# Performance work log

Measured on AMD Instinct MI355X. Metric: run time of the kernel, lower is better.

## Reference

```python
import jax, jax.numpy as jnp
import numpy as np

H = 128
M = 50000
L = 400000
EPS = 1e-9


def setup_inputs() -> dict:
    key = jax.random.key(0)
    ks = jax.random.split(key, 24)
    d = {
        'x_emb': jax.random.normal(ks[0], (M, H), jnp.float32),
        'child_h': jax.random.normal(ks[1], (M, H), jnp.float32),
        'child_c': jax.random.normal(ks[2], (M, H), jnp.float32),
        'pair_cand_idx': jax.random.randint(ks[3], (L,), 0, M, jnp.int32),
        'pair_child_idx': jax.random.randint(ks[4], (L,), 0, M, jnp.int32),
    }
    s = 1.0 / np.sqrt(H)
    names = ['Wi_w', 'Ui_w', 'Wf_w', 'Uf_w', 'Wo_w', 'Uo_w', 'Wc_w', 'Uc_w', 'Wa_w', 'Ua_w']
    for i, n in enumerate(names):
        d[n] = jax.random.uniform(ks[5 + i], (H, H), jnp.float32, -s, s)
    for i, n in enumerate(['Wi_b', 'Wf_b', 'Wo_b', 'Wc_b', 'Wa_b']):
        d[n] = jax.random.uniform(ks[15 + i], (H,), jnp.float32, -s, s)
    d['v_w'] = jax.random.uniform(ks[20], (H,), jnp.float32, -s, s)
    return d


def reference(x_emb, child_h, child_c, pair_cand_idx, pair_child_idx,
              Wi_w, Ui_w, Wf_w, Uf_w, Wo_w, Uo_w, Wc_w, Uc_w, Wa_w, Ua_w,
              Wi_b, Wf_b, Wo_b, Wc_b, Wa_b, v_w):
    m = x_emb.shape[0]
    ci, chi = pair_cand_idx, pair_child_idx

    # --- segment attention (torch version runs under no_grad) ---
    Ah = child_h @ Wa_w.T + Wa_b          # [M,H]
    Bx = x_emb @ Ua_w.T                   # [M,H]
    e = jnp.tanh(Ah[chi] + Bx[ci]) @ v_w  # [L]
    seg_max = jax.ops.segment_max(e, ci, num_segments=m)
    x_exp = jnp.exp(e - seg_max[ci])
    seg_sum = jax.ops.segment_sum(x_exp, ci, num_segments=m) + EPS
    attn = x_exp / seg_sum[ci]            # [L]
    h_hat = jax.ops.segment_sum(attn[:, None] * child_h[chi], ci, num_segments=m)  # [M,H]

    # --- tree-LSTM gates ---
    i_j = jax.nn.sigmoid(x_emb @ Wi_w.T + Wi_b + h_hat @ Ui_w.T)
    Wfx = x_emb @ Wf_w.T + Wf_b
    Ufh = child_h @ Uf_w.T
    f_pair = jax.nn.sigmoid(Wfx[ci] + Ufh[chi])                       # [L,H]
    sum_f_c = jax.ops.segment_sum(f_pair * child_c[chi], ci, num_segments=m)
    c_t = jnp.tanh(x_emb @ Wc_w.T + Wc_b + h_hat @ Uc_w.T)
    c = i_j * c_t + sum_f_c
    o_j = jax.nn.sigmoid(x_emb @ Wo_w.T + Wo_b + h_hat @ Uo_w.T)
    h = o_j * jnp.tanh(c)
    return (h, c)
```

## Files before the change

### kernel.cpp

```cpp
#include <hip/hip_runtime.h>
#include <cstdint>
#include <cstddef>

#define H 128
#define PSTRIDE 512

typedef __bf16 v8bf __attribute__((ext_vector_type(8)));
typedef __bf16 v4bf __attribute__((ext_vector_type(4)));
typedef float  v4f  __attribute__((ext_vector_type(4)));

__device__ __forceinline__ float ftanh(float x) {
    return 1.f - 2.f / (1.f + __expf(2.f * x));
}
__device__ __forceinline__ float fsigm(float x) {
    return 1.f / (1.f + __expf(-x));
}

struct MatDesc {
    const __bf16* A;
    int           lda;
    const __bf16* Wb;
    const float*  bias;
    __bf16*       C;
    int           ldc;
};
struct MatBatch { MatDesc m[7]; };
struct WPtrs { const float* w[10]; };

__global__ __launch_bounds__(256) void prep_k(WPtrs wp, __bf16* __restrict__ Wb,
                                              const float* __restrict__ x,
                                              const float* __restrict__ chh,
                                              const float* __restrict__ chc,
                                              __bf16* __restrict__ xe,
                                              __bf16* __restrict__ P,
                                              const int* __restrict__ ci,
                                              int* __restrict__ counts,
                                              int MH4, int L) {
    int tid = blockIdx.x * 256 + threadIdx.x;
    if (tid < 40960) {
        int mat = tid >> 12;
        int off = (tid & 4095) << 2;
        v4f a = *(const v4f*)(wp.w[mat] + off);
        v4bf b;
#pragma unroll
        for (int k = 0; k < 4; ++k) b[k] = (__bf16)a[k];
        *(v4bf*)(Wb + mat * 16384 + off) = b;
        return;
    }
    int i = tid - 40960;
    if (i < MH4) {
        v4f a = ((const v4f*)x)[i];
        v4f b = ((const v4f*)chh)[i];
        v4f c = ((const v4f*)chc)[i];
        v4bf ab, bb, cb;
#pragma unroll
        for (int k = 0; k < 4; ++k) {
            ab[k] = (__bf16)a[k]; bb[k] = (__bf16)b[k]; cb[k] = (__bf16)c[k];
        }
        ((v4bf*)xe)[i] = ab;
        int m = i >> 5;
        int q = (i & 31) << 2;
        __bf16* prow = P + (size_t)m * PSTRIDE + q;
        *(v4bf*)prow = bb;
        *(v4bf*)(prow + H) = cb;
        return;
    }
    int l = i - MH4;
    if (l < L) atomicAdd(&counts[ci[l]], 1);
}

__global__ __launch_bounds__(256) void gemm_batch(MatBatch batch, int M) {
    const MatDesc d = batch.m[blockIdx.y];
    __shared__ __bf16 wlds[H][H + 8];

    for (int t = threadIdx.x; t < 2048; t += 256) {
        int n = t >> 4;
        int k = (t & 15) << 3;
        *(v8bf*)&wlds[n][k] = *(const v8bf*)(d.Wb + n * H + k);
    }
    __syncthreads();

    const int wave = threadIdx.x >> 6;
    const int lane = threadIdx.x & 63;
    const int quad = lane >> 4;
    const int l16  = lane & 15;
    const int r0   = blockIdx.x * 128 + wave * 32;

    v4f acc0[8], acc1[8];
#pragma unroll
    for (int nt = 0; nt < 8; ++nt) {
        acc0[nt] = (v4f){0.f, 0.f, 0.f, 0.f};
        acc1[nt] = (v4f){0.f, 0.f, 0.f, 0.f};
    }

    const __bf16* ar0 = d.A + (size_t)(r0 + l16) * d.lda + quad * 8;
    const __bf16* ar1 = d.A + (size_t)(r0 + 16 + l16) * d.lda + quad * 8;
#pragma unroll
    for (int k0 = 0; k0 < H; k0 += 32) {
        v8bf a0 = *(const v8bf*)(ar0 + k0);
        v8bf a1 = *(const v8bf*)(ar1 + k0);
#pragma unroll
        for (int nt = 0; nt < 8; ++nt) {
            v8bf b = *(const v8bf*)(&wlds[nt * 16 + l16][k0 + quad * 8]);
            acc0[nt] = __builtin_amdgcn_mfma_f32_16x16x32_bf16(a0, b, acc0[nt], 0, 0, 0);
            acc1[nt] = __builtin_amdgcn_mfma_f32_16x16x32_bf16(a1, b, acc1[nt], 0, 0, 0);
        }
    }

#pragma unroll
    for (int nt = 0; nt < 8; ++nt) {
        int n = nt * 16 + l16;
        float bia = d.bias ? d.bias[n] : 0.f;
#pragma unroll
        for (int r = 0; r < 4; ++r) {
            int m0 = r0 + quad * 4 + r;
            int m1 = m0 + 16;
            if (m0 < M) d.C[(size_t)m0 * d.ldc + n] = (__bf16)(acc0[nt][r] + bia);
            if (m1 < M) d.C[(size_t)m1 * d.ldc + n] = (__bf16)(acc1[nt][r] + bia);
        }
    }
}

__global__ __launch_bounds__(1024) void scan_local(const int* __restrict__ counts,
                                                   int* __restrict__ excl,
                                                   int* __restrict__ bsums, int M) {
    __shared__ int s[1024];
    int tid = threadIdx.x;
    int idx = blockIdx.x * 1024 + tid;
    int v = (idx < M) ? counts[idx] : 0;
    s[tid] = v;
    __syncthreads();
    for (int off = 1; off < 1024; off <<= 1) {
        int t = (tid >= off) ? s[tid - off] : 0;
        __syncthreads();
        s[tid] += t;
        __syncthreads();
    }
    if (idx < M) excl[idx] = s[tid] - v;
    if (tid == 1023) bsums[blockIdx.x] = s[1023];
}

__global__ __launch_bounds__(1024) void scan_fused(int* __restrict__ rowptr,
                                                   int* __restrict__ cursor,
                                                   const int* __restrict__ bsums,
                                                   const int* __restrict__ counts,
                                                   int M, int nb) {
    __shared__ int s[1024];
    int t = threadIdx.x, b = blockIdx.x;
    int v = (t < nb) ? bsums[t] : 0;
    s[t] = v;
    __syncthreads();
    for (int off = 1; off < 1024; off <<= 1) {
        int tt = (t >= off) ? s[t - off] : 0;
        __syncthreads();
        s[t] += tt;
        __syncthreads();
    }
    int boff = (b == 0) ? 0 : s[b - 1];
    int idx = b * 1024 + t;
    if (idx < M) {
        int val = rowptr[idx] + boff;
        rowptr[idx] = val;
        cursor[idx] = val;
        if (idx == M - 1) rowptr[M] = val + counts[M - 1];
    }
}

__global__ __launch_bounds__(256) void scatter_k(const int* __restrict__ ci,
                                                 const int* __restrict__ chi,
                                                 int* __restrict__ cursor,
                                                 int* __restrict__ payload, int L) {
    int l = blockIdx.x * 256 + threadIdx.x;
    if (l < L) {
        int pos = atomicAdd(&cursor[ci[l]], 1);
        payload[pos] = chi[l];
    }
}

__global__ __launch_bounds__(128) void segment_fused(const int* __restrict__ rowptr,
                                                     const int* __restrict__ payload,
                                                     const float* __restrict__ vw,
                                                     const __bf16* __restrict__ Bx,
                                                     const __bf16* __restrict__ Wfx,
                                                     const __bf16* __restrict__ P,
                                                     __bf16* __restrict__ hhat,
                                                     float* __restrict__ sumfc, int M) {
    int wl   = threadIdx.x & 63;
    int half = wl & 32;
    int l32  = wl & 31;
    int m = blockIdx.x * 4 + (threadIdx.x >> 5);
    if (m >= M) return;
    int start = rowptr[m], deg = rowptr[m + 1] - start;
    int h = l32 << 2;

    v4bf bx4 = *(const v4bf*)(Bx + (size_t)m * H + h);
    v4bf wf4 = *(const v4bf*)(Wfx + (size_t)m * H + h);
    v4f  vv  = *(const v4f*)(vw + h);
    float bxf[4], wff[4];
#pragma unroll
    for (int k = 0; k < 4; ++k) { bxf[k] = (float)bx4[k]; wff[k] = (float)wf4[k]; }

    int pl0 = (l32 < deg) ? payload[start + l32] : 0;
    int pl1 = (32 + l32 < deg) ? payload[start + 32 + l32] : 0;

    int jcap = deg < 64 ? deg : 64;
    float e0 = 0.f, e1 = 0.f, denom = 0.f;

    for (int j = 0; j < jcap; ++j) {
        int cj = __shfl((j & 32) ? pl1 : pl0, half | (j & 31), 64);
        v4bf a4 = *(const v4bf*)(P + (size_t)cj * PSTRIDE + 3 * H + h);
        float s = 0.f;
#pragma unroll
        for (int k = 0; k < 4; ++k) s += ftanh((float)a4[k] + bxf[k]) * vv[k];
        s += __shfl_xor(s, 1);
        s += __shfl_xor(s, 2);
        s += __shfl_xor(s, 4);
        s += __shfl_xor(s, 8);
        s += __shfl_xor(s, 16);
        float ex = __expf(s);
        denom += ex;
        if (l32 == (j & 31)) { if (j & 32) e1 = ex; else e0 = ex; }
    }
    for (int j = 64; j < deg; ++j) {
        int cj = payload[start + j];
        v4bf a4 = *(const v4bf*)(P + (size_t)cj * PSTRIDE + 3 * H + h);
        float s = 0.f;
#pragma unroll
        for (int k = 0; k < 4; ++k) s += ftanh((float)a4[k] + bxf[k]) * vv[k];
        s += __shfl_xor(s, 1);
        s += __shfl_xor(s, 2);
        s += __shfl_xor(s, 4);
        s += __shfl_xor(s, 8);
        s += __shfl_xor(s, 16);
        denom += __expf(s);
    }
    float inv = 1.f / (denom + 1e-9f);

    float acch[4] = {0.f, 0.f, 0.f, 0.f};
    float accf[4] = {0.f, 0.f, 0.f, 0.f};
#pragma unroll 2
    for (int j = 0; j < jcap; ++j) {
        int src = half | (j & 31);
        int   cj = __shfl((j & 32) ? pl1 : pl0, src, 64);
        float ex = __shfl((j & 32) ? e1 : e0, src, 64);
        float a = ex * inv;
        const __bf16* pb = P + (size_t)cj * PSTRIDE + h;
        v4bf h4 = *(const v4bf*)pb;
        v4bf c4 = *(const v4bf*)(pb + H);
        v4bf u4 = *(const v4bf*)(pb + 2 * H);
#pragma unroll
        for (int k = 0; k < 4; ++k) {
            acch[k] += a * (float)h4[k];
            accf[k] += fsigm(wff[k] + (float)u4[k]) * (float)c4[k];
        }
    }
    for (int j = 64; j < deg; ++j) {
        int cj = payload[start + j];
        const __bf16* pb = P + (size_t)cj * PSTRIDE + h;
        v4bf a4 = *(const v4bf*)(pb + 3 * H);
        float s = 0.f;
#pragma unroll
        for (int k = 0; k < 4; ++k) s += ftanh((float)a4[k] + bxf[k]) * vv[k];
        s += __shfl_xor(s, 1);
        s += __shfl_xor(s, 2);
        s += __shfl_xor(s, 4);
        s += __shfl_xor(s, 8);
        s += __shfl_xor(s, 16);
        float a = __expf(s) * inv;
        v4bf h4 = *(const v4bf*)pb;
        v4bf c4 = *(const v4bf*)(pb + H);
        v4bf u4 = *(const v4bf*)(pb + 2 * H);
#pragma unroll
        for (int k = 0; k < 4; ++k) {
            acch[k] += a * (float)h4[k];
            accf[k] += fsigm(wff[k] + (float)u4[k]) * (float)c4[k];
        }
    }

    v4bf hb;
    v4f sf;
#pragma unroll
    for (int k = 0; k < 4; ++k) { hb[k] = (__bf16)acch[k]; sf[k] = accf[k]; }
    *(v4bf*)(hhat + (size_t)m * H + h) = hb;
    *(v4f*)(sumfc + (size_t)m * H + h) = sf;
}

__global__ __launch_bounds__(256) void final_k(const __bf16* __restrict__ Xi, const __bf16* __restrict__ Hi,
                                               const __bf16* __restrict__ Xc, const __bf16* __restrict__ Hc,
                                               const __bf16* __restrict__ Xo, const __bf16* __restrict__ Ho,
                                               const float* __restrict__ sumfc,
                                               float* __restrict__ out, int MH4, int MH) {
    int i = blockIdx.x * 256 + threadIdx.x;
    if (i >= MH4) return;
    v4bf xi = ((const v4bf*)Xi)[i], hi = ((const v4bf*)Hi)[i];
    v4bf xc = ((const v4bf*)Xc)[i], hc = ((const v4bf*)Hc)[i];
    v4bf xo = ((const v4bf*)Xo)[i], ho = ((const v4bf*)Ho)[i];
    v4f sf = ((const v4f*)sumfc)[i];
    v4f hout, cout;
#pragma unroll
    for (int k = 0; k < 4; ++k) {
        float ig = fsigm((float)xi[k] + (float)hi[k]);
        float ct = ftanh((float)xc[k] + (float)hc[k]);
        float og = fsigm((float)xo[k] + (float)ho[k]);
        float c = ig * ct + sf[k];
        cout[k] = c;
        hout[k] = og * ftanh(c);
    }
    ((v4f*)out)[i] = hout;
    ((v4f*)(out + MH))[i] = cout;
}

extern "C" void kernel_launch(void* const* d_in, const int* in_sizes, int n_in,
                              void* d_out, int out_size, void* d_ws, size_t ws_size,
                              hipStream_t stream) {
    const float* x_emb   = (const float*)d_in[0];
    const float* child_h = (const float*)d_in[1];
    const float* child_c = (const float*)d_in[2];
    const int*   ci      = (const int*)d_in[3];
    const int*   chi     = (const int*)d_in[4];
    const float* Wi_b = (const float*)d_in[15];
    const float* Wf_b = (const float*)d_in[16];
    const float* Wo_b = (const float*)d_in[17];
    const float* Wc_b = (const float*)d_in[18];
    const float* Wa_b = (const float*)d_in[19];
    const float* vw   = (const float*)d_in[20];

    const int M    = in_sizes[0] / H;
    const int L    = in_sizes[3];
    const int Mpad = (M + 127) & ~127;
    const int MH   = M * H;
    const int MH4  = MH / 4;

    char* p = (char*)d_ws;
    auto alloc = [&](size_t bytes) {
        char* r = p;
        p += (bytes + 255) & ~(size_t)255;
        return (void*)r;
    };
    size_t bfbytes = (size_t)Mpad * H * sizeof(__bf16);
    __bf16* xe16   = (__bf16*)alloc(bfbytes);
    __bf16* P      = (__bf16*)alloc((size_t)Mpad * PSTRIDE * sizeof(__bf16));
    __bf16* hhat16 = (__bf16*)alloc(bfbytes);
    __bf16* Bx16   = (__bf16*)alloc(bfbytes);
    __bf16* Wfx16  = (__bf16*)alloc(bfbytes);
    __bf16* Xi16   = (__bf16*)alloc(bfbytes);
    __bf16* Xc16   = (__bf16*)alloc(bfbytes);
    __bf16* Xo16   = (__bf16*)alloc(bfbytes);
    __bf16* Wb     = (__bf16*)alloc(10 * 16384 * sizeof(__bf16));
    float* sumfc   = (float*)alloc((size_t)MH * 4);
    int*   payload = (int*)alloc((size_t)L * 4);
    int*   counts  = (int*)alloc((size_t)M * 4);
    int*   rowptr  = (int*)alloc((size_t)(M + 1) * 4);
    int*   cursor  = (int*)alloc((size_t)M * 4);
    int*   bsums   = (int*)alloc(1024 * 4);
    __bf16* Hi16 = Bx16;
    __bf16* Hc16 = Wfx16;
    __bf16* Ho16 = P;

    hipMemsetAsync(counts, 0, (size_t)M * 4, stream);

    WPtrs wp;
    for (int k = 0; k < 10; ++k) wp.w[k] = (const float*)d_in[5 + k];
    int prep_items = 40960 + MH4 + L;
    prep_k<<<(prep_items + 255) / 256, 256, 0, stream>>>(wp, Wb, x_emb, child_h, child_c,
                                                         xe16, P, ci, counts, MH4, L);

    const __bf16* Wi = Wb + 0 * 16384;
    const __bf16* Ui = Wb + 1 * 16384;
    const __bf16* Wf = Wb + 2 * 16384;
    const __bf16* Uf = Wb + 3 * 16384;
    const __bf16* Wo = Wb + 4 * 16384;
    const __bf16* Uo = Wb + 5 * 16384;
    const __bf16* Wc = Wb + 6 * 16384;
    const __bf16* Uc = Wb + 7 * 16384;
    const __bf16* Wa = Wb + 8 * 16384;
    const __bf16* Ua = Wb + 9 * 16384;

    MatBatch ba{};
    ba.m[0] = MatDesc{P,    PSTRIDE, Wa, Wa_b,    P + 3 * H, PSTRIDE};
    ba.m[1] = MatDesc{xe16, H,       Ua, nullptr, Bx16,      H};
    ba.m[2] = MatDesc{xe16, H,       Wf, Wf_b,    Wfx16,     H};
    ba.m[3] = MatDesc{P,    PSTRIDE, Uf, nullptr, P + 2 * H, PSTRIDE};
    ba.m[4] = MatDesc{xe16, H,       Wi, Wi_b,    Xi16,      H};
    ba.m[5] = MatDesc{xe16, H,       Wc, Wc_b,    Xc16,      H};
    ba.m[6] = MatDesc{xe16, H,       Wo, Wo_b,    Xo16,      H};
    dim3 gA(Mpad / 128, 7);
    gemm_batch<<<gA, 256, 0, stream>>>(ba, M);

    int nb = (M + 1023) / 1024;
    scan_local<<<nb, 1024, 0, stream>>>(counts, rowptr, bsums, M);
    scan_fused<<<nb, 1024, 0, stream>>>(rowptr, cursor, bsums, counts, M, nb);

    scatter_k<<<(L + 255) / 256, 256, 0, stream>>>(ci, chi, cursor, payload, L);

    segment_fused<<<(M + 3) / 4, 128, 0, stream>>>(rowptr, payload, vw, Bx16, Wfx16, P,
                                                   hhat16, sumfc, M);

    MatBatch bb{};
    bb.m[0] = MatDesc{hhat16, H, Ui, nullptr, Hi16, H};
    bb.m[1] = MatDesc{hhat16, H, Uc, nullptr, Hc16, H};
    bb.m[2] = MatDesc{hhat16, H, Uo, nullptr, Ho16, H};
    dim3 gB(Mpad / 128, 3);
    gemm_batch<<<gB, 256, 0, stream>>>(bb, M);

    final_k<<<(MH4 + 255) / 256, 256, 0, stream>>>(Xi16, Hi16, Xc16, Hc16, Xo16, Ho16, sumfc,
                                                   (float*)d_out, MH4, MH);
}
```

Measured before the change: 402.0 us.

## Share A tiles across grouped GEMMs and process two children per wave in segment kernel

The batched GEMM now groups all matrices that share an input. Each block loads its A rows into registers once and loops over several weight matrices, double-buffering the next weight in LDS, instead of reloading A for every matrix in a separate block. The segment attention kernel now has each half-wave of 16 lanes handle a different child with 8-wide bf16 loads, so two pairs are processed per iteration. The half-wave partial sums are combined with a cross-half shuffle at the end. This cuts redundant A traffic and serial iteration count, at the cost of fewer GEMM blocks (less parallelism), more registers, and masked wasted work when the degree is odd.

```diff
diff --git a/kernel.cpp b/kernel.cpp
--- a/kernel.cpp
+++ b/kernel.cpp
@@ -16,15 +16,16 @@
     return 1.f / (1.f + __expf(-x));
 }
 
-struct MatDesc {
+struct GDesc {
     const __bf16* A;
     int           lda;
-    const __bf16* Wb;
-    const float*  bias;
-    __bf16*       C;
-    int           ldc;
+    int           nm;
+    const __bf16* W[5];
+    const float*  bias[5];
+    __bf16*       C[5];
+    int           ldc[5];
 };
-struct MatBatch { MatDesc m[7]; };
+struct GBatch { GDesc g[2]; };
 struct WPtrs { const float* w[10]; };
 
 __global__ __launch_bounds__(256) void prep_k(WPtrs wp, __bf16* __restrict__ Wb,
@@ -69,16 +70,9 @@
     if (l < L) atomicAdd(&counts[ci[l]], 1);
 }
 
-__global__ __launch_bounds__(256) void gemm_batch(MatBatch batch, int M) {
-    const MatDesc d = batch.m[blockIdx.y];
-    __shared__ __bf16 wlds[H][H + 8];
-
-    for (int t = threadIdx.x; t < 2048; t += 256) {
-        int n = t >> 4;
-        int k = (t & 15) << 3;
-        *(v8bf*)&wlds[n][k] = *(const v8bf*)(d.Wb + n * H + k);
-    }
-    __syncthreads();
+__global__ __launch_bounds__(256) void gemm_group(GBatch gb, int M) {
+    const GDesc d = gb.g[blockIdx.y];
+    __shared__ __bf16 wlds[2][H][H + 8];
 
     const int wave = threadIdx.x >> 6;
     const int lane = threadIdx.x & 63;
@@ -86,38 +80,74 @@
     const int l16  = lane & 15;
     const int r0   = blockIdx.x * 128 + wave * 32;
 
-    v4f acc0[8], acc1[8];
-#pragma unroll
-    for (int nt = 0; nt < 8; ++nt) {
-        acc0[nt] = (v4f){0.f, 0.f, 0.f, 0.f};
-        acc1[nt] = (v4f){0.f, 0.f, 0.f, 0.f};
-    }
-
+#pragma unroll
+    for (int i = 0; i < 8; ++i) {
+        int c = threadIdx.x + 256 * i;
+        int n = c >> 4, k = (c & 15) << 3;
+        *(v8bf*)&wlds[0][n][k] = *(const v8bf*)(d.W[0] + n * H + k);
+    }
+
+    v8bf afr0[4], afr1[4];
     const __bf16* ar0 = d.A + (size_t)(r0 + l16) * d.lda + quad * 8;
-    const __bf16* ar1 = d.A + (size_t)(r0 + 16 + l16) * d.lda + quad * 8;
-#pragma unroll
-    for (int k0 = 0; k0 < H; k0 += 32) {
-        v8bf a0 = *(const v8bf*)(ar0 + k0);
-        v8bf a1 = *(const v8bf*)(ar1 + k0);
+    const __bf16* ar1 = ar0 + (size_t)16 * d.lda;
+#pragma unroll
+    for (int kc = 0; kc < 4; ++kc) {
+        afr0[kc] = *(const v8bf*)(ar0 + kc * 32);
+        afr1[kc] = *(const v8bf*)(ar1 + kc * 32);
+    }
+    __syncthreads();
+
+    for (int mat = 0; mat < d.nm; ++mat) {
+        int cur = mat & 1;
+        v8bf pf[8];
+        if (mat + 1 < d.nm) {
+#pragma unroll
+            for (int i = 0; i < 8; ++i) {
+                int c = threadIdx.x + 256 * i;
+                pf[i] = *(const v8bf*)(d.W[mat + 1] + (c >> 4) * H + ((c & 15) << 3));
+            }
+        }
+
+        v4f acc0[8], acc1[8];
 #pragma unroll
         for (int nt = 0; nt < 8; ++nt) {
-            v8bf b = *(const v8bf*)(&wlds[nt * 16 + l16][k0 + quad * 8]);
-            acc0[nt] = __builtin_amdgcn_mfma_f32_16x16x32_bf16(a0, b, acc0[nt], 0, 0, 0);
-            acc1[nt] = __builtin_amdgcn_mfma_f32_16x16x32_bf16(a1, b, acc1[nt], 0, 0, 0);
-        }
-    }
-
-#pragma unroll
-    for (int nt = 0; nt < 8; ++nt) {
-        int n = nt * 16 + l16;
-        float bia = d.bias ? d.bias[n] : 0.f;
-#pragma unroll
-        for (int r = 0; r < 4; ++r) {
-            int m0 = r0 + quad * 4 + r;
-            int m1 = m0 + 16;
-            if (m0 < M) d.C[(size_t)m0 * d.ldc + n] = (__bf16)(acc0[nt][r] + bia);
-            if (m1 < M) d.C[(size_t)m1 * d.ldc + n] = (__bf16)(acc1[nt][r] + bia);
-        }
+            acc0[nt] = (v4f){0.f, 0.f, 0.f, 0.f};
+            acc1[nt] = (v4f){0.f, 0.f, 0.f, 0.f};
+        }
+#pragma unroll
+        for (int kc = 0; kc < 4; ++kc) {
+#pragma unroll
+            for (int nt = 0; nt < 8; ++nt) {
+                v8bf b = *(const v8bf*)(&wlds[cur][nt * 16 + l16][kc * 32 + quad * 8]);
+                acc0[nt] = __builtin_amdgcn_mfma_f32_16x16x32_bf16(afr0[kc], b, acc0[nt], 0, 0, 0);
+                acc1[nt] = __builtin_amdgcn_mfma_f32_16x16x32_bf16(afr1[kc], b, acc1[nt], 0, 0, 0);
+            }
+        }
+
+        __bf16* Cm = d.C[mat];
+        const float* bp = d.bias[mat];
+        int ldc = d.ldc[mat];
+#pragma unroll
+        for (int nt = 0; nt < 8; ++nt) {
+            int n = nt * 16 + l16;
+            float bia = bp ? bp[n] : 0.f;
+#pragma unroll
+            for (int r = 0; r < 4; ++r) {
+                int m0 = r0 + quad * 4 + r;
+                int m1 = m0 + 16;
+                if (m0 < M) Cm[(size_t)m0 * ldc + n] = (__bf16)(acc0[nt][r] + bia);
+                if (m1 < M) Cm[(size_t)m1 * ldc + n] = (__bf16)(acc1[nt][r] + bia);
+            }
+        }
+
+        if (mat + 1 < d.nm) {
+#pragma unroll
+            for (int i = 0; i < 8; ++i) {
+                int c = threadIdx.x + 256 * i;
+                *(v8bf*)&wlds[cur ^ 1][c >> 4][(c & 15) << 3] = pf[i];
+            }
+        }
+        __syncthreads();
     }
 }
 
@@ -185,104 +215,127 @@
                                                      const __bf16* __restrict__ P,
                                                      __bf16* __restrict__ hhat,
                                                      float* __restrict__ sumfc, int M) {
-    int wl   = threadIdx.x & 63;
-    int half = wl & 32;
-    int l32  = wl & 31;
-    int m = blockIdx.x * 4 + (threadIdx.x >> 5);
+    const int wl   = threadIdx.x & 63;
+    const int half = wl & 32;
+    const int l32  = wl & 31;
+    const int sg   = l32 >> 4;
+    const int s16  = l32 & 15;
+    const int h8   = s16 << 3;
+    const int m = blockIdx.x * 4 + (threadIdx.x >> 5);
     if (m >= M) return;
-    int start = rowptr[m], deg = rowptr[m + 1] - start;
-    int h = l32 << 2;
-
-    v4bf bx4 = *(const v4bf*)(Bx + (size_t)m * H + h);
-    v4bf wf4 = *(const v4bf*)(Wfx + (size_t)m * H + h);
-    v4f  vv  = *(const v4f*)(vw + h);
-    float bxf[4], wff[4];
-#pragma unroll
-    for (int k = 0; k < 4; ++k) { bxf[k] = (float)bx4[k]; wff[k] = (float)wf4[k]; }
+    const int start = rowptr[m];
+    const int deg   = rowptr[m + 1] - start;
+
+    v8bf bx8 = *(const v8bf*)(Bx + (size_t)m * H + h8);
+    v8bf wf8 = *(const v8bf*)(Wfx + (size_t)m * H + h8);
+    v4f vva = *(const v4f*)(vw + h8);
+    v4f vvb = *(const v4f*)(vw + h8 + 4);
+    float bxf[8], wff[8], vvf[8];
+#pragma unroll
+    for (int k = 0; k < 8; ++k) {
+        bxf[k] = (float)bx8[k];
+        wff[k] = (float)wf8[k];
+        vvf[k] = (k < 4) ? vva[k] : vvb[k - 4];
+    }
 
     int pl0 = (l32 < deg) ? payload[start + l32] : 0;
     int pl1 = (32 + l32 < deg) ? payload[start + 32 + l32] : 0;
 
-    int jcap = deg < 64 ? deg : 64;
+    const int jcap  = deg < 64 ? deg : 64;
+    const int iters = (jcap + 1) >> 1;
+
     float e0 = 0.f, e1 = 0.f, denom = 0.f;
 
-    for (int j = 0; j < jcap; ++j) {
-        int cj = __shfl((j & 32) ? pl1 : pl0, half | (j & 31), 64);
-        v4bf a4 = *(const v4bf*)(P + (size_t)cj * PSTRIDE + 3 * H + h);
+    for (int it = 0; it < iters; ++it) {
+        int j = 2 * it + sg;
+        int src = half | (j & 31);
+        int cj = __shfl((it >= 16) ? pl1 : pl0, src, 64);
+        v8bf a8 = *(const v8bf*)(P + (size_t)cj * PSTRIDE + 3 * H + h8);
         float s = 0.f;
 #pragma unroll
-        for (int k = 0; k < 4; ++k) s += ftanh((float)a4[k] + bxf[k]) * vv[k];
+        for (int k = 0; k < 8; ++k) s += ftanh((float)a8[k] + bxf[k]) * vvf[k];
         s += __shfl_xor(s, 1);
         s += __shfl_xor(s, 2);
         s += __shfl_xor(s, 4);
         s += __shfl_xor(s, 8);
-        s += __shfl_xor(s, 16);
-        float ex = __expf(s);
+        float ex = (j < jcap) ? __expf(s) : 0.f;
         denom += ex;
-        if (l32 == (j & 31)) { if (j & 32) e1 = ex; else e0 = ex; }
-    }
-    for (int j = 64; j < deg; ++j) {
+        if ((it & 15) == s16) { if (it & 16) e1 = ex; else e0 = ex; }
+    }
+    for (int j = 64 + sg; j < deg; j += 2) {
         int cj = payload[start + j];
-        v4bf a4 = *(const v4bf*)(P + (size_t)cj * PSTRIDE + 3 * H + h);
+        v8bf a8 = *(const v8bf*)(P + (size_t)cj * PSTRIDE + 3 * H + h8);
         float s = 0.f;
 #pragma unroll
-        for (int k = 0; k < 4; ++k) s += ftanh((float)a4[k] + bxf[k]) * vv[k];
+        for (int k = 0; k < 8; ++k) s += ftanh((float)a8[k] + bxf[k]) * vvf[k];
         s += __shfl_xor(s, 1);
         s += __shfl_xor(s, 2);
         s += __shfl_xor(s, 4);
         s += __shfl_xor(s, 8);
-        s += __shfl_xor(s, 16);
         denom += __expf(s);
     }
+    denom += __shfl_xor(denom, 16);
     float inv = 1.f / (denom + 1e-9f);
 
-    float acch[4] = {0.f, 0.f, 0.f, 0.f};
-    float accf[4] = {0.f, 0.f, 0.f, 0.f};
-#pragma unroll 2
-    for (int j = 0; j < jcap; ++j) {
+    float acch[8] = {0.f, 0.f, 0.f, 0.f, 0.f, 0.f, 0.f, 0.f};
+    float accf[8] = {0.f, 0.f, 0.f, 0.f, 0.f, 0.f, 0.f, 0.f};
+    for (int it = 0; it < iters; ++it) {
+        int j = 2 * it + sg;
         int src = half | (j & 31);
-        int   cj = __shfl((j & 32) ? pl1 : pl0, src, 64);
-        float ex = __shfl((j & 32) ? e1 : e0, src, 64);
-        float a = ex * inv;
-        const __bf16* pb = P + (size_t)cj * PSTRIDE + h;
-        v4bf h4 = *(const v4bf*)pb;
-        v4bf c4 = *(const v4bf*)(pb + H);
-        v4bf u4 = *(const v4bf*)(pb + 2 * H);
-#pragma unroll
-        for (int k = 0; k < 4; ++k) {
+        int cj = __shfl((it >= 16) ? pl1 : pl0, src, 64);
+        int esrc = half | (sg << 4) | (it & 15);
+        float exj = __shfl((it & 16) ? e1 : e0, esrc, 64);
+        float msk = (j < jcap) ? 1.f : 0.f;
+        float a = exj * inv * msk;
+        const __bf16* pb = P + (size_t)cj * PSTRIDE + h8;
+        v8bf h4 = *(const v8bf*)pb;
+        v8bf c4 = *(const v8bf*)(pb + H);
+        v8bf u4 = *(const v8bf*)(pb + 2 * H);
+#pragma unroll
+        for (int k = 0; k < 8; ++k) {
             acch[k] += a * (float)h4[k];
-            accf[k] += fsigm(wff[k] + (float)u4[k]) * (float)c4[k];
-        }
-    }
-    for (int j = 64; j < deg; ++j) {
+            accf[k] += msk * fsigm(wff[k] + (float)u4[k]) * (float)c4[k];
+        }
+    }
+    for (int j = 64 + sg; j < deg; j += 2) {
         int cj = payload[start + j];
-        const __bf16* pb = P + (size_t)cj * PSTRIDE + h;
-        v4bf a4 = *(const v4bf*)(pb + 3 * H);
+        const __bf16* pb = P + (size_t)cj * PSTRIDE + h8;
+        v8bf a8 = *(const v8bf*)(pb + 3 * H);
         float s = 0.f;
 #pragma unroll
-        for (int k = 0; k < 4; ++k) s += ftanh((float)a4[k] + bxf[k]) * vv[k];
+        for (int k = 0; k < 8; ++k) s += ftanh((float)a8[k] + bxf[k]) * vvf[k];
         s += __shfl_xor(s, 1);
         s += __shfl_xor(s, 2);
         s += __shfl_xor(s, 4);
         s += __shfl_xor(s, 8);
-        s += __shfl_xor(s, 16);
         float a = __expf(s) * inv;
-        v4bf h4 = *(const v4bf*)pb;
-        v4bf c4 = *(const v4bf*)(pb + H);
-        v4bf u4 = *(const v4bf*)(pb + 2 * H);
-#pragma unroll
-        for (int k = 0; k < 4; ++k) {
+        v8bf h4 = *(const v8bf*)pb;
+        v8bf c4 = *(const v8bf*)(pb + H);
+        v8bf u4 = *(const v8bf*)(pb + 2 * H);
+#pragma unroll
+        for (int k = 0; k < 8; ++k) {
             acch[k] += a * (float)h4[k];
             accf[k] += fsigm(wff[k] + (float)u4[k]) * (float)c4[k];
         }
     }
 
-    v4bf hb;
-    v4f sf;
-#pragma unroll
-    for (int k = 0; k < 4; ++k) { hb[k] = (__bf16)acch[k]; sf[k] = accf[k]; }
-    *(v4bf*)(hhat + (size_t)m * H + h) = hb;
-    *(v4f*)(sumfc + (size_t)m * H + h) = sf;
+#pragma unroll
+    for (int k = 0; k < 8; ++k) {
+        acch[k] += __shfl_xor(acch[k], 16);
+        accf[k] += __shfl_xor(accf[k], 16);
+    }
+    if (l32 < 16) {
+        v8bf hb;
+        v4f sfa, sfb;
+#pragma unroll
+        for (int k = 0; k < 8; ++k) {
+            hb[k] = (__bf16)acch[k];
+            if (k < 4) sfa[k] = accf[k]; else sfb[k - 4] = accf[k];
+        }
+        *(v8bf*)(hhat + (size_t)m * H + h8) = hb;
+        *(v4f*)(sumfc + (size_t)m * H + h8) = sfa;
+        *(v4f*)(sumfc + (size_t)m * H + h8 + 4) = sfb;
+    }
 }
 
 __global__ __launch_bounds__(256) void final_k(const __bf16* __restrict__ Xi, const __bf16* __restrict__ Hi,
@@ -376,16 +429,18 @@
     const __bf16* Wa = Wb + 8 * 16384;
     const __bf16* Ua = Wb + 9 * 16384;
 
-    MatBatch ba{};
-    ba.m[0] = MatDesc{P,    PSTRIDE, Wa, Wa_b,    P + 3 * H, PSTRIDE};
-    ba.m[1] = MatDesc{xe16, H,       Ua, nullptr, Bx16,      H};
-    ba.m[2] = MatDesc{xe16, H,       Wf, Wf_b,    Wfx16,     H};
-    ba.m[3] = MatDesc{P,    PSTRIDE, Uf, nullptr, P + 2 * H, PSTRIDE};
-    ba.m[4] = MatDesc{xe16, H,       Wi, Wi_b,    Xi16,      H};
-    ba.m[5] = MatDesc{xe16, H,       Wc, Wc_b,    Xc16,      H};
-    ba.m[6] = MatDesc{xe16, H,       Wo, Wo_b,    Xo16,      H};
-    dim3 gA(Mpad / 128, 7);
-    gemm_batch<<<gA, 256, 0, stream>>>(ba, M);
+    GBatch ga{};
+    ga.g[0].A = xe16; ga.g[0].lda = H; ga.g[0].nm = 5;
+    ga.g[0].W[0] = Ua; ga.g[0].bias[0] = nullptr; ga.g[0].C[0] = Bx16;  ga.g[0].ldc[0] = H;
+    ga.g[0].W[1] = Wf; ga.g[0].bias[1] = Wf_b;    ga.g[0].C[1] = Wfx16; ga.g[0].ldc[1] = H;
+    ga.g[0].W[2] = Wi; ga.g[0].bias[2] = Wi_b;    ga.g[0].C[2] = Xi16;  ga.g[0].ldc[2] = H;
+    ga.g[0].W[3] = Wc; ga.g[0].bias[3] = Wc_b;    ga.g[0].C[3] = Xc16;  ga.g[0].ldc[3] = H;
+    ga.g[0].W[4] = Wo; ga.g[0].bias[4] = Wo_b;    ga.g[0].C[4] = Xo16;  ga.g[0].ldc[4] = H;
+    ga.g[1].A = P; ga.g[1].lda = PSTRIDE; ga.g[1].nm = 2;
+    ga.g[1].W[0] = Wa; ga.g[1].bias[0] = Wa_b;    ga.g[1].C[0] = P + 3 * H; ga.g[1].ldc[0] = PSTRIDE;
+    ga.g[1].W[1] = Uf; ga.g[1].bias[1] = nullptr; ga.g[1].C[1] = P + 2 * H; ga.g[1].ldc[1] = PSTRIDE;
+    dim3 gA(Mpad / 128, 2);
+    gemm_group<<<gA, 256, 0, stream>>>(ga, M);
 
     int nb = (M + 1023) / 1024;
     scan_local<<<nb, 1024, 0, stream>>>(counts, rowptr, bsums, M);
@@ -396,12 +451,13 @@
     segment_fused<<<(M + 3) / 4, 128, 0, stream>>>(rowptr, payload, vw, Bx16, Wfx16, P,
                                                    hhat16, sumfc, M);
 
-    MatBatch bb{};
-    bb.m[0] = MatDesc{hhat16, H, Ui, nullptr, Hi16, H};
-    bb.m[1] = MatDesc{hhat16, H, Uc, nullptr, Hc16, H};
-    bb.m[2] = MatDesc{hhat16, H, Uo, nullptr, Ho16, H};
-    dim3 gB(Mpad / 128, 3);
-    gemm_batch<<<gB, 256, 0, stream>>>(bb, M);
+    GBatch gbb{};
+    gbb.g[0].A = hhat16; gbb.g[0].lda = H; gbb.g[0].nm = 3;
+    gbb.g[0].W[0] = Ui; gbb.g[0].bias[0] = nullptr; gbb.g[0].C[0] = Hi16; gbb.g[0].ldc[0] = H;
+    gbb.g[0].W[1] = Uc; gbb.g[0].bias[1] = nullptr; gbb.g[0].C[1] = Hc16; gbb.g[0].ldc[1] = H;
+    gbb.g[0].W[2] = Uo; gbb.g[0].bias[2] = nullptr; gbb.g[0].C[2] = Ho16; gbb.g[0].ldc[2] = H;
+    dim3 gB(Mpad / 128, 1);
+    gemm_group<<<gB, 256, 0, stream>>>(gbb, M);
 
     final_k<<<(MH4 + 255) / 256, 256, 0, stream>>>(Xi16, Hi16, Xc16, Hc16, Xo16, Ho16, sumfc,
                                                    (float*)d_out, MH4, MH);
```

Result: slower. 443.7 us (+10.4%).
